# Kernel tuning notes

Measured on AMD Instinct MI355X. Metric: run time of the kernel, lower is better.

## Reference

```python
import jax, jax.numpy as jnp
import numpy as np
import math

B, W, BINS, BANDS = 2, 2048, 1024, 8  # cropsize == W
HEAD = BINS // BANDS


def setup_inputs() -> dict:
    key = jax.random.key(0)
    ks = jax.random.split(key, 10)
    s = 1.0 / math.sqrt(BINS)
    return {
        "x": jax.random.normal(ks[0], (B, W, BINS), jnp.float32),
        "Wq": jax.random.normal(ks[1], (BINS, BINS), jnp.float32) * s,
        "bq": jax.random.normal(ks[2], (BINS,), jnp.float32) * s,
        "Wk": jax.random.normal(ks[3], (BINS, BINS), jnp.float32) * s,
        "bk": jax.random.normal(ks[4], (BINS,), jnp.float32) * s,
        "Wv": jax.random.normal(ks[5], (BINS, BINS), jnp.float32) * s,
        "bv": jax.random.normal(ks[6], (BINS,), jnp.float32) * s,
        "Wo": jax.random.normal(ks[7], (BINS, BINS), jnp.float32) * s,
        "bo": jax.random.normal(ks[8], (BINS,), jnp.float32) * s,
        "er": jax.random.normal(ks[9], (HEAD, W), jnp.float32) * s,  # [bins//num_bands, cropsize]
    }


def reference(x, Wq, bq, Wk, bk, Wv, bv, Wo, bo, er):
    b, w, h = x.shape
    n = BANDS
    # projections -> [b, n, w, head]
    q = (x @ Wq.T + bq).reshape(b, w, n, -1).transpose(0, 2, 1, 3)
    k = (x @ Wk.T + bk).reshape(b, w, n, -1).transpose(0, 2, 1, 3)
    v = (x @ Wv.T + bv).reshape(b, w, n, -1).transpose(0, 2, 1, 3)
    # relative position bias via skew trick: [b, n, w, cropsize]
    qer = jnp.einsum('bnwd,dc->bnwc', q, er)
    p = jnp.pad(qer, ((0, 0), (0, 0), (0, 0), (1, 0)))  # pad left of last dim
    p = jnp.swapaxes(p, 2, 3)[:, :, 1:, :]              # [b, n, w, w]
    a = (jnp.einsum('bnqd,bnkd->bnqk', q, k) + p) / math.sqrt(h)
    attn = jax.nn.softmax(a, axis=-1)
    ctx = jnp.einsum('bnqk,bnkd->bnqd', attn, v).transpose(0, 2, 1, 3).reshape(b, w, h)
    o = ctx @ Wo.T + bo
    return (o, a)
```

## Files before the change

kernel.cpp:

```cpp
#include <hip/hip_runtime.h>

typedef __attribute__((ext_vector_type(8))) __bf16 bf16x8;
typedef __attribute__((ext_vector_type(4))) float f32x4;

__device__ __forceinline__ unsigned short f2bf(float f) {
  __bf16 h = (__bf16)f;
  return __builtin_bit_cast(unsigned short, h);
}

__device__ __forceinline__ f32x4 mfma_bf16(bf16x8 a, bf16x8 b, f32x4 c) {
  return __builtin_amdgcn_mfma_f32_16x16x32_bf16(a, b, c, 0, 0, 0);
}

__device__ __forceinline__ void gload_lds16(const void* g, void* l) {
  __builtin_amdgcn_global_load_lds((const __attribute__((address_space(1))) void*)g,
                                   (__attribute__((address_space(3))) void*)l, 16, 0, 0);
}


__global__ void cvt_f32_bf16(const float* __restrict__ in, unsigned short* __restrict__ out, int n4) {
  int i = blockIdx.x * blockDim.x + threadIdx.x;
  if (i < n4) {
    float4 v = reinterpret_cast<const float4*>(in)[i];
    ushort4 o;
    o.x = f2bf(v.x); o.y = f2bf(v.y); o.z = f2bf(v.z); o.w = f2bf(v.w);
    reinterpret_cast<ushort4*>(out)[i] = o;
  }
}

__global__ void cvt4_f32_bf16(const float* __restrict__ a, const float* __restrict__ b,
                              const float* __restrict__ c, const float* __restrict__ d,
                              unsigned short* __restrict__ oa, unsigned short* __restrict__ ob,
                              unsigned short* __restrict__ oc, unsigned short* __restrict__ od) {
  int i = blockIdx.x * blockDim.x + threadIdx.x;
  int which = i >> 18, j = i & 262143;
  const float* src = (which == 0) ? a : (which == 1) ? b : (which == 2) ? c : d;
  unsigned short* dst = (which == 0) ? oa : (which == 1) ? ob : (which == 2) ? oc : od;
  float4 v = reinterpret_cast<const float4*>(src)[j];
  ushort4 o;
  o.x = f2bf(v.x); o.y = f2bf(v.y); o.z = f2bf(v.z); o.w = f2bf(v.w);
  reinterpret_cast<ushort4*>(dst)[j] = o;
}

__global__ void er_transpose(const float* __restrict__ er, unsigned short* __restrict__ ert) {
  __shared__ float t[32][33];
  int w0 = blockIdx.x * 32, d0 = blockIdx.y * 32;
  int tx = threadIdx.x, ty = threadIdx.y;
#pragma unroll
  for (int i = 0; i < 4; ++i)
    t[ty + i * 8][tx] = er[(size_t)(d0 + ty + i * 8) * 2048 + w0 + tx];
  __syncthreads();
#pragma unroll
  for (int i = 0; i < 4; ++i)
    ert[(size_t)(w0 + ty + i * 8) * 128 + d0 + tx] = f2bf(t[tx][ty + i * 8]);
}


__device__ __forceinline__ void gemm_tile(
    const unsigned short* __restrict__ A,
    const unsigned short* __restrict__ Bt,
    const float* __restrict__ bias,
    void* __restrict__ C,
    int mode, int i0, int j0,
    unsigned short* lds)
{
  char* base = (char*)lds;

  const int tid = threadIdx.x;
  const int lane = tid & 63, wid = tid >> 6;
  const int lr = lane & 15, lq = lane >> 4;
  const int wr = wid >> 1, wc = wid & 1;

  f32x4 acc[4][4] = {};

  const int srow = tid >> 2;
  const int scolb = (tid & 3) << 4;

  const char* Abase = (const char*)A + (size_t)(i0 + srow) * 2048 + scolb;
  const char* Bbase = (const char*)Bt + (size_t)(j0 + srow) * 2048 + scolb;

  gload_lds16(Abase,             base + tid * 16);
  gload_lds16(Abase + 64 * 2048, base + 4096 + tid * 16);
  gload_lds16(Bbase,             base + 8192 + tid * 16);
  gload_lds16(Bbase + 64 * 2048, base + 12288 + tid * 16);

  for (int kt = 0; kt < 32; ++kt) {
    char* cbuf = base + (kt & 1) * 16384;
    char* nbuf = base + ((kt + 1) & 1) * 16384;

    asm volatile("s_waitcnt vmcnt(0)" ::: "memory");
    __builtin_amdgcn_sched_barrier(0);
    __builtin_amdgcn_s_barrier();
    __builtin_amdgcn_sched_barrier(0);

    if (kt < 31) {
      const int k0b = (kt + 1) * 64;
      gload_lds16(Abase + k0b,             nbuf + tid * 16);
      gload_lds16(Abase + k0b + 64 * 2048, nbuf + 4096 + tid * 16);
      gload_lds16(Bbase + k0b,             nbuf + 8192 + tid * 16);
      gload_lds16(Bbase + k0b + 64 * 2048, nbuf + 12288 + tid * 16);
    }
    __builtin_amdgcn_sched_barrier(0);

    bf16x8 af[4], bfr[4];
#pragma unroll
    for (int m = 0; m < 4; ++m)
      af[m] = *(const bf16x8*)(cbuf + (wr * 64 + m * 16 + lr) * 64 + lq * 16);
#pragma unroll
    for (int n = 0; n < 4; ++n)
      bfr[n] = *(const bf16x8*)(cbuf + 8192 + (wc * 64 + n * 16 + lr) * 64 + lq * 16);
    __builtin_amdgcn_s_setprio(1);
#pragma unroll
    for (int m = 0; m < 4; ++m)
#pragma unroll
      for (int n = 0; n < 4; ++n)
        acc[m][n] = mfma_bf16(af[m], bfr[n], acc[m][n]);
    __builtin_amdgcn_s_setprio(0);
  }

  float bv[4];
#pragma unroll
  for (int n = 0; n < 4; ++n) bv[n] = bias[j0 + wc * 64 + n * 16 + lr];

  if (mode == 1) {
    __syncthreads();
#pragma unroll
    for (int m = 0; m < 4; ++m)
#pragma unroll
      for (int n = 0; n < 4; ++n)
#pragma unroll
        for (int r = 0; r < 4; ++r) {
          int il = wr * 64 + m * 16 + lq * 4 + r;
          int jl = wc * 64 + n * 16 + lr;
          lds[jl * 132 + il] = f2bf(acc[m][n][r] + bv[n]);
        }
    __syncthreads();
    const int b = i0 >> 11, w0 = i0 & 2047, bd = j0 >> 7;
    unsigned short* out = (unsigned short*)C;
    for (int idx = tid; idx < 16384; idx += 256) {
      int dl = idx >> 7, wl = idx & 127;
      out[(size_t)((b * 8 + bd) * 128 + dl) * 2048 + w0 + wl] = lds[dl * 132 + wl];
    }
  } else if (mode == 0) {
    unsigned short* out = (unsigned short*)C;
#pragma unroll
    for (int m = 0; m < 4; ++m)
#pragma unroll
      for (int n = 0; n < 4; ++n)
#pragma unroll
        for (int r = 0; r < 4; ++r) {
          int gi = i0 + wr * 64 + m * 16 + lq * 4 + r;
          int gj = j0 + wc * 64 + n * 16 + lr;
          out[(size_t)gi * 1024 + gj] = f2bf(acc[m][n][r] + bv[n]);
        }
  } else {
    float* out = (float*)C;
#pragma unroll
    for (int m = 0; m < 4; ++m)
#pragma unroll
      for (int n = 0; n < 4; ++n)
#pragma unroll
        for (int r = 0; r < 4; ++r) {
          int gi = i0 + wr * 64 + m * 16 + lq * 4 + r;
          int gj = j0 + wc * 64 + n * 16 + lr;
          out[(size_t)gi * 1024 + gj] = acc[m][n][r] + bv[n];
        }
  }
}

__global__ __launch_bounds__(256, 2) void gemm_qkv(
    const unsigned short* __restrict__ xb,
    const unsigned short* __restrict__ Wqb, const unsigned short* __restrict__ Wkb,
    const unsigned short* __restrict__ Wvb,
    const float* __restrict__ bq, const float* __restrict__ bk, const float* __restrict__ bv_,
    unsigned short* __restrict__ Qb, unsigned short* __restrict__ Kb,
    unsigned short* __restrict__ Vtb)
{
  __shared__ unsigned short lds[16896];
  const int which = blockIdx.y >> 3;
  const int i0 = blockIdx.x * 128, j0 = (blockIdx.y & 7) * 128;
  const unsigned short* Bt = (which == 0) ? Wqb : (which == 1) ? Wkb : Wvb;
  const float* bias = (which == 0) ? bq : (which == 1) ? bk : bv_;
  void* C = (which == 0) ? (void*)Qb : (which == 1) ? (void*)Kb : (void*)Vtb;
  gemm_tile(xb, Bt, bias, C, (which == 2) ? 1 : 0, i0, j0, lds);
}

__global__ __launch_bounds__(256, 2) void gemm_bt(
    const unsigned short* __restrict__ A,
    const unsigned short* __restrict__ Bt,
    const float* __restrict__ bias,
    void* __restrict__ C,
    int mode)
{
  __shared__ unsigned short lds[16896];
  gemm_tile(A, Bt, bias, C, mode, blockIdx.x * 128, blockIdx.y * 128, lds);
}


__global__ __launch_bounds__(512) void attn_fused(
    const unsigned short* __restrict__ Qb,
    const unsigned short* __restrict__ Kb,
    const unsigned short* __restrict__ Vt,
    const unsigned short* __restrict__ ErT,
    float* __restrict__ a_out,
    unsigned short* __restrict__ ctx)
{
  __shared__ __align__(16) char Klb[32768];
  __shared__ __align__(16) char Qlb[32768];
  __shared__ __align__(16) char Vlb[32768];
  __shared__ __align__(16) char Plb[32768];

  const int bb = blockIdx.x;
  const int bd = bb & 7, b = bb >> 3;
  const int qi0 = blockIdx.y * 128;
  const int tid = threadIdx.x, wid = tid >> 6, lane = tid & 63;
  const int lr = lane & 15, lq = lane >> 4;

  bf16x8 qf[4], ef[4];
  {
    const unsigned short* Qrow = Qb + (size_t)(b * 2048 + qi0 + wid * 16 + lr) * 1024 + bd * 128;
    const unsigned short* Erow = ErT + (size_t)(qi0 + wid * 16 + lr) * 128;
#pragma unroll
    for (int kk = 0; kk < 4; ++kk) {
      qf[kk] = *(const bf16x8*)(Qrow + kk * 32 + lq * 8);
      ef[kk] = *(const bf16x8*)(Erow + kk * 32 + lq * 8);
    }
  }

  int ldso[4];
  const char *ksrc[4], *qsrc[4], *vsrc[4];
#pragma unroll
  for (int p = 0; p < 4; ++p) {
    int L = p * 8192 + tid * 16;
    int row = L >> 8, cs = L & 255;
    int sc = cs ^ ((row & 7) << 4);
    ldso[p] = L;
    ksrc[p] = (const char*)Kb + ((size_t)(b * 2048 + row) * 1024 + bd * 128) * 2 + sc;
    qsrc[p] = (const char*)Qb + ((size_t)(b * 2048 + row) * 1024 + bd * 128) * 2 + sc;
    vsrc[p] = (const char*)Vt + ((size_t)(bb * 128 + row) * 2048) * 2 + sc;
  }

#pragma unroll
  for (int p = 0; p < 4; ++p) gload_lds16(ksrc[p], Klb + ldso[p]);
#pragma unroll
  for (int p = 0; p < 4; ++p) gload_lds16(qsrc[p], Qlb + ldso[p]);
#pragma unroll
  for (int p = 0; p < 4; ++p) gload_lds16(vsrc[p], Vlb + ldso[p]);

  f32x4 oacc[8] = {};
  float M[4], L[4];
#pragma unroll
  for (int r = 0; r < 4; ++r) { M[r] = -1e30f; L[r] = 0.f; }

  float* abase = a_out + (size_t)bb * 2048 * 2048;

  for (int kt = 0; kt < 16; ++kt) {
    const int kj0 = kt * 128;
    const size_t nkq = (size_t)((kt + 1) & 15) * 262144;
    const size_t nv = (size_t)((kt + 1) & 15) * 256;

    asm volatile("s_waitcnt vmcnt(4)" ::: "memory");
    __builtin_amdgcn_sched_barrier(0);
    __builtin_amdgcn_s_barrier();
    __builtin_amdgcn_sched_barrier(0);

    f32x4 sacc[8] = {};
    __builtin_amdgcn_s_setprio(1);
#pragma unroll
    for (int kk = 0; kk < 4; ++kk) {
#pragma unroll
      for (int nf = 0; nf < 8; ++nf) {
        const int row = nf * 16 + lr;
        bf16x8 kf = *(const bf16x8*)(Klb + row * 256 + ((kk * 64 + lq * 16) ^ ((row & 7) << 4)));
        sacc[nf] = mfma_bf16(qf[kk], kf, sacc[nf]);
      }
#pragma unroll
      for (int nf = 0; nf < 8; ++nf) {
        const int row = nf * 16 + lr;
        bf16x8 qkf = *(const bf16x8*)(Qlb + row * 256 + ((kk * 64 + lq * 16) ^ ((row & 7) << 4)));
        sacc[nf] = mfma_bf16(ef[kk], qkf, sacc[nf]);
      }
    }
    __builtin_amdgcn_s_setprio(0);

    __builtin_amdgcn_sched_barrier(0);
    __builtin_amdgcn_s_barrier();
    __builtin_amdgcn_sched_barrier(0);

#pragma unroll
    for (int nf = 0; nf < 8; ++nf)
#pragma unroll
      for (int r = 0; r < 4; ++r) sacc[nf][r] *= 0.03125f;
    {
      const int qrow_base = qi0 + wid * 16 + lq * 4;
#pragma unroll
      for (int nf = 0; nf < 8; ++nf)
#pragma unroll
        for (int r = 0; r < 4; ++r)
          abase[(size_t)(qrow_base + r) * 2048 + kj0 + nf * 16 + lr] = sacc[nf][r];
    }

    __builtin_amdgcn_sched_barrier(0);
#pragma unroll
    for (int p = 0; p < 4; ++p) gload_lds16(ksrc[p] + nkq, Klb + ldso[p]);
#pragma unroll
    for (int p = 0; p < 4; ++p) gload_lds16(qsrc[p] + nkq, Qlb + ldso[p]);
    __builtin_amdgcn_sched_barrier(0);

    float rmax[4];
#pragma unroll
    for (int r = 0; r < 4; ++r) {
      float m0 = sacc[0][r];
#pragma unroll
      for (int nf = 1; nf < 8; ++nf) m0 = fmaxf(m0, sacc[nf][r]);
      m0 = fmaxf(m0, __shfl_xor(m0, 1));
      m0 = fmaxf(m0, __shfl_xor(m0, 2));
      m0 = fmaxf(m0, __shfl_xor(m0, 4));
      m0 = fmaxf(m0, __shfl_xor(m0, 8));
      rmax[r] = m0;
    }
    bool small = (rmax[0] - M[0] <= 8.f) & (rmax[1] - M[1] <= 8.f) &
                 (rmax[2] - M[2] <= 8.f) & (rmax[3] - M[3] <= 8.f);
    unsigned long long vote = __ballot(small);
    if (vote != ~0ull) {
      float scl[4];
#pragma unroll
      for (int r = 0; r < 4; ++r) {
        float Mn = fmaxf(M[r], rmax[r]);
        scl[r] = __expf(M[r] - Mn);
        M[r] = Mn;
        L[r] *= scl[r];
      }
#pragma unroll
      for (int dn = 0; dn < 8; ++dn)
#pragma unroll
        for (int r = 0; r < 4; ++r) oacc[dn][r] *= scl[r];
    }
    float rsum[4] = {0.f, 0.f, 0.f, 0.f};
#pragma unroll
    for (int nf = 0; nf < 8; ++nf)
#pragma unroll
      for (int r = 0; r < 4; ++r) {
        float pv = __expf(sacc[nf][r] - M[r]);
        sacc[nf][r] = pv;
        rsum[r] += pv;
      }
    {
      const int prow0 = wid * 16 + lq * 4;
#pragma unroll
      for (int nf = 0; nf < 8; ++nf)
#pragma unroll
        for (int r = 0; r < 4; ++r) {
          const int row = prow0 + r;
          *(unsigned short*)(Plb + row * 256 + (((nf * 16 + lr) * 2) ^ ((row & 7) << 4))) =
              f2bf(sacc[nf][r]);
        }
    }
#pragma unroll
    for (int r = 0; r < 4; ++r) {
      rsum[r] += __shfl_xor(rsum[r], 1);
      rsum[r] += __shfl_xor(rsum[r], 2);
      rsum[r] += __shfl_xor(rsum[r], 4);
      rsum[r] += __shfl_xor(rsum[r], 8);
      L[r] += rsum[r];
    }

    asm volatile("s_waitcnt vmcnt(8)" ::: "memory");
    __builtin_amdgcn_sched_barrier(0);

    __builtin_amdgcn_s_setprio(1);
#pragma unroll
    for (int kk = 0; kk < 4; ++kk) {
      const int prow = wid * 16 + lr;
      bf16x8 pf = *(const bf16x8*)(Plb + prow * 256 + ((kk * 64 + lq * 16) ^ ((prow & 7) << 4)));
#pragma unroll
      for (int dn = 0; dn < 8; ++dn) {
        const int vrow = dn * 16 + lr;
        bf16x8 vf = *(const bf16x8*)(Vlb + vrow * 256 + ((kk * 64 + lq * 16) ^ ((vrow & 7) << 4)));
        oacc[dn] = mfma_bf16(pf, vf, oacc[dn]);
      }
    }
    __builtin_amdgcn_s_setprio(0);

    __builtin_amdgcn_sched_barrier(0);
    __builtin_amdgcn_s_barrier();
    __builtin_amdgcn_sched_barrier(0);
#pragma unroll
    for (int p = 0; p < 4; ++p) gload_lds16(vsrc[p] + nv, Vlb + ldso[p]);
    __builtin_amdgcn_sched_barrier(0);
  }

  {
    const int qrow_base = b * 2048 + qi0 + wid * 16 + lq * 4;
#pragma unroll
    for (int dn = 0; dn < 8; ++dn)
#pragma unroll
      for (int r = 0; r < 4; ++r) {
        float v = oacc[dn][r] / L[r];
        ctx[(size_t)(qrow_base + r) * 1024 + bd * 128 + dn * 16 + lr] = f2bf(v);
      }
  }
}


extern "C" void kernel_launch(void* const* d_in, const int* in_sizes, int n_in,
                              void* d_out, int out_size, void* d_ws, size_t ws_size,
                              hipStream_t stream) {
  const float* x  = (const float*)d_in[0];
  const float* Wq = (const float*)d_in[1];
  const float* bq = (const float*)d_in[2];
  const float* Wk = (const float*)d_in[3];
  const float* bk = (const float*)d_in[4];
  const float* Wv = (const float*)d_in[5];
  const float* bv = (const float*)d_in[6];
  const float* Wo = (const float*)d_in[7];
  const float* bo = (const float*)d_in[8];
  const float* er = (const float*)d_in[9];

  char* ws = (char*)d_ws;
  unsigned short* xb  = (unsigned short*)(ws + 0);
  unsigned short* Wqb = (unsigned short*)(ws + 8388608);
  unsigned short* Wkb = (unsigned short*)(ws + 10485760);
  unsigned short* Wvb = (unsigned short*)(ws + 12582912);
  unsigned short* Wob = (unsigned short*)(ws + 14680064);
  unsigned short* Qb  = (unsigned short*)(ws + 16777216);
  unsigned short* Kb  = (unsigned short*)(ws + 25165824);
  unsigned short* Vtb = (unsigned short*)(ws + 33554432);
  unsigned short* ctx = (unsigned short*)(ws + 41943040);
  unsigned short* ert = (unsigned short*)(ws + 50331648);

  float* a_out = (float*)d_out + 4194304;

  cvt_f32_bf16<<<dim3(4096), dim3(256), 0, stream>>>(x, xb, 1048576);
  cvt4_f32_bf16<<<dim3(4096), dim3(256), 0, stream>>>(Wq, Wk, Wv, Wo, Wqb, Wkb, Wvb, Wob);
  er_transpose<<<dim3(64, 4), dim3(32, 8), 0, stream>>>(er, ert);

  gemm_qkv<<<dim3(32, 24), dim3(256), 0, stream>>>(xb, Wqb, Wkb, Wvb, bq, bk, bv,
                                                   Qb, Kb, Vtb);

  attn_fused<<<dim3(16, 16), dim3(512), 0, stream>>>(Qb, Kb, Vtb, ert, a_out, ctx);

  gemm_bt<<<dim3(32, 8), dim3(256), 0, stream>>>(ctx, Wob, bo, d_out, 2);
}
```

Measured before the change: 188.6 us.

## Split attention over key halves with 32-row warps and add merge kernel

Each attention block now handles 256 query rows (32 per warp, two MFMA fragments) over one half of the keys. This doubles reuse of each K/Q/V LDS tile per load, and LDS use is cut by sharing one buffer between K/Q and P. Partial outputs and per-row max/sum are written to workspace, and a new merge kernel combines the two halves into ctx. The cost is an extra kernel launch, an extra bf16 round trip of partial outputs, and loss of the earlier cross-iteration prefetch overlap, since loads now wait with vmcnt(0) and are issued only after PV. Register pressure also rises.

After: 322.0 us, median of 3. 1.71x slower.

```diff
diff --git a/kernel.cpp b/kernel.cpp
--- a/kernel.cpp
+++ b/kernel.cpp
@@ -6,6 +6,11 @@
 __device__ __forceinline__ unsigned short f2bf(float f) {
   __bf16 h = (__bf16)f;
   return __builtin_bit_cast(unsigned short, h);
+}
+
+__device__ __forceinline__ float bf2f(unsigned short u) {
+  unsigned int x = ((unsigned int)u) << 16;
+  return __builtin_bit_cast(float, x);
 }
 
 __device__ __forceinline__ f32x4 mfma_bf16(bf16x8 a, bf16x8 b, f32x4 c) {
@@ -203,27 +208,30 @@
     const unsigned short* __restrict__ Vt,
     const unsigned short* __restrict__ ErT,
     float* __restrict__ a_out,
-    unsigned short* __restrict__ ctx)
+    unsigned short* __restrict__ Opart,
+    float* __restrict__ MLp)
 {
-  __shared__ __align__(16) char Klb[32768];
-  __shared__ __align__(16) char Qlb[32768];
+  __shared__ __align__(16) char KQlb[65536];
   __shared__ __align__(16) char Vlb[32768];
-  __shared__ __align__(16) char Plb[32768];
 
   const int bb = blockIdx.x;
   const int bd = bb & 7, b = bb >> 3;
-  const int qi0 = blockIdx.y * 128;
+  const int qt = blockIdx.y >> 1, kh = blockIdx.y & 1;
+  const int qi0 = qt * 256;
+  const int kbase = kh * 1024;
   const int tid = threadIdx.x, wid = tid >> 6, lane = tid & 63;
   const int lr = lane & 15, lq = lane >> 4;
 
-  bf16x8 qf[4], ef[4];
-  {
-    const unsigned short* Qrow = Qb + (size_t)(b * 2048 + qi0 + wid * 16 + lr) * 1024 + bd * 128;
-    const unsigned short* Erow = ErT + (size_t)(qi0 + wid * 16 + lr) * 128;
+  bf16x8 qf[2][4], ef[2][4];
+#pragma unroll
+  for (int fr = 0; fr < 2; ++fr) {
+    const unsigned short* Qrow =
+        Qb + (size_t)(b * 2048 + qi0 + wid * 32 + fr * 16 + lr) * 1024 + bd * 128;
+    const unsigned short* Erow = ErT + (size_t)(qi0 + wid * 32 + fr * 16 + lr) * 128;
 #pragma unroll
     for (int kk = 0; kk < 4; ++kk) {
-      qf[kk] = *(const bf16x8*)(Qrow + kk * 32 + lq * 8);
-      ef[kk] = *(const bf16x8*)(Erow + kk * 32 + lq * 8);
+      qf[fr][kk] = *(const bf16x8*)(Qrow + kk * 32 + lq * 8);
+      ef[fr][kk] = *(const bf16x8*)(Erow + kk * 32 + lq * 8);
     }
   }
 
@@ -231,153 +239,153 @@
   const char *ksrc[4], *qsrc[4], *vsrc[4];
 #pragma unroll
   for (int p = 0; p < 4; ++p) {
-    int L = p * 8192 + tid * 16;
-    int row = L >> 8, cs = L & 255;
+    int Lo = p * 8192 + tid * 16;
+    int row = Lo >> 8, cs = Lo & 255;
     int sc = cs ^ ((row & 7) << 4);
-    ldso[p] = L;
-    ksrc[p] = (const char*)Kb + ((size_t)(b * 2048 + row) * 1024 + bd * 128) * 2 + sc;
-    qsrc[p] = (const char*)Qb + ((size_t)(b * 2048 + row) * 1024 + bd * 128) * 2 + sc;
-    vsrc[p] = (const char*)Vt + ((size_t)(bb * 128 + row) * 2048) * 2 + sc;
-  }
-
-#pragma unroll
-  for (int p = 0; p < 4; ++p) gload_lds16(ksrc[p], Klb + ldso[p]);
-#pragma unroll
-  for (int p = 0; p < 4; ++p) gload_lds16(qsrc[p], Qlb + ldso[p]);
+    ldso[p] = Lo;
+    ksrc[p] = (const char*)Kb + ((size_t)(b * 2048 + kbase + row) * 1024 + bd * 128) * 2 + sc;
+    qsrc[p] = (const char*)Qb + ((size_t)(b * 2048 + kbase + row) * 1024 + bd * 128) * 2 + sc;
+    vsrc[p] = (const char*)Vt + ((size_t)(bb * 128 + row) * 2048 + kbase) * 2 + sc;
+  }
+#pragma unroll
+  for (int p = 0; p < 4; ++p) gload_lds16(ksrc[p], KQlb + ldso[p]);
+#pragma unroll
+  for (int p = 0; p < 4; ++p) gload_lds16(qsrc[p], KQlb + 32768 + ldso[p]);
 #pragma unroll
   for (int p = 0; p < 4; ++p) gload_lds16(vsrc[p], Vlb + ldso[p]);
 
-  f32x4 oacc[8] = {};
-  float M[4], L[4];
-#pragma unroll
-  for (int r = 0; r < 4; ++r) { M[r] = -1e30f; L[r] = 0.f; }
-
-  float* abase = a_out + (size_t)bb * 2048 * 2048;
-
-  for (int kt = 0; kt < 16; ++kt) {
-    const int kj0 = kt * 128;
-    const size_t nkq = (size_t)((kt + 1) & 15) * 262144;
-    const size_t nv = (size_t)((kt + 1) & 15) * 256;
-
-    asm volatile("s_waitcnt vmcnt(4)" ::: "memory");
+  f32x4 oacc[2][8] = {};
+  float M[2][4], Ls[2][4];
+#pragma unroll
+  for (int fr = 0; fr < 2; ++fr)
+#pragma unroll
+    for (int r = 0; r < 4; ++r) { M[fr][r] = -1e30f; Ls[fr][r] = 0.f; }
+
+  float* abase = a_out + (size_t)bb * 4194304;
+
+  for (int kt = 0; kt < 8; ++kt) {
+    asm volatile("s_waitcnt vmcnt(0)" ::: "memory");
     __builtin_amdgcn_sched_barrier(0);
     __builtin_amdgcn_s_barrier();
     __builtin_amdgcn_sched_barrier(0);
 
-    f32x4 sacc[8] = {};
+    f32x4 sacc[2][8] = {};
     __builtin_amdgcn_s_setprio(1);
 #pragma unroll
     for (int kk = 0; kk < 4; ++kk) {
 #pragma unroll
       for (int nf = 0; nf < 8; ++nf) {
         const int row = nf * 16 + lr;
-        bf16x8 kf = *(const bf16x8*)(Klb + row * 256 + ((kk * 64 + lq * 16) ^ ((row & 7) << 4)));
-        sacc[nf] = mfma_bf16(qf[kk], kf, sacc[nf]);
+        const int coff = (kk * 64 + lq * 16) ^ ((row & 7) << 4);
+        bf16x8 kf = *(const bf16x8*)(KQlb + row * 256 + coff);
+        sacc[0][nf] = mfma_bf16(qf[0][kk], kf, sacc[0][nf]);
+        sacc[1][nf] = mfma_bf16(qf[1][kk], kf, sacc[1][nf]);
+        bf16x8 qkf = *(const bf16x8*)(KQlb + 32768 + row * 256 + coff);
+        sacc[0][nf] = mfma_bf16(ef[0][kk], qkf, sacc[0][nf]);
+        sacc[1][nf] = mfma_bf16(ef[1][kk], qkf, sacc[1][nf]);
       }
-#pragma unroll
-      for (int nf = 0; nf < 8; ++nf) {
-        const int row = nf * 16 + lr;
-        bf16x8 qkf = *(const bf16x8*)(Qlb + row * 256 + ((kk * 64 + lq * 16) ^ ((row & 7) << 4)));
-        sacc[nf] = mfma_bf16(ef[kk], qkf, sacc[nf]);
+    }
+    __builtin_amdgcn_s_setprio(0);
+
+    __builtin_amdgcn_sched_barrier(0);
+    __builtin_amdgcn_s_barrier();
+    __builtin_amdgcn_sched_barrier(0);
+
+    const int kcol0 = kbase + kt * 128;
+#pragma unroll
+    for (int fr = 0; fr < 2; ++fr) {
+#pragma unroll
+      for (int nf = 0; nf < 8; ++nf)
+#pragma unroll
+        for (int r = 0; r < 4; ++r) sacc[fr][nf][r] *= 0.03125f;
+      const int qrow_base = qi0 + wid * 32 + fr * 16 + lq * 4;
+#pragma unroll
+      for (int nf = 0; nf < 8; ++nf)
+#pragma unroll
+        for (int r = 0; r < 4; ++r)
+          abase[(size_t)(qrow_base + r) * 2048 + kcol0 + nf * 16 + lr] = sacc[fr][nf][r];
+    }
+
+    float rmax[2][4];
+#pragma unroll
+    for (int fr = 0; fr < 2; ++fr)
+#pragma unroll
+      for (int r = 0; r < 4; ++r) {
+        float m0 = sacc[fr][0][r];
+#pragma unroll
+        for (int nf = 1; nf < 8; ++nf) m0 = fmaxf(m0, sacc[fr][nf][r]);
+        m0 = fmaxf(m0, __shfl_xor(m0, 1));
+        m0 = fmaxf(m0, __shfl_xor(m0, 2));
+        m0 = fmaxf(m0, __shfl_xor(m0, 4));
+        m0 = fmaxf(m0, __shfl_xor(m0, 8));
+        rmax[fr][r] = m0;
       }
-    }
-    __builtin_amdgcn_s_setprio(0);
-
-    __builtin_amdgcn_sched_barrier(0);
-    __builtin_amdgcn_s_barrier();
-    __builtin_amdgcn_sched_barrier(0);
-
-#pragma unroll
-    for (int nf = 0; nf < 8; ++nf)
-#pragma unroll
-      for (int r = 0; r < 4; ++r) sacc[nf][r] *= 0.03125f;
-    {
-      const int qrow_base = qi0 + wid * 16 + lq * 4;
-#pragma unroll
-      for (int nf = 0; nf < 8; ++nf)
-#pragma unroll
-        for (int r = 0; r < 4; ++r)
-          abase[(size_t)(qrow_base + r) * 2048 + kj0 + nf * 16 + lr] = sacc[nf][r];
-    }
-
-    __builtin_amdgcn_sched_barrier(0);
-#pragma unroll
-    for (int p = 0; p < 4; ++p) gload_lds16(ksrc[p] + nkq, Klb + ldso[p]);
-#pragma unroll
-    for (int p = 0; p < 4; ++p) gload_lds16(qsrc[p] + nkq, Qlb + ldso[p]);
-    __builtin_amdgcn_sched_barrier(0);
-
-    float rmax[4];
-#pragma unroll
-    for (int r = 0; r < 4; ++r) {
-      float m0 = sacc[0][r];
-#pragma unroll
-      for (int nf = 1; nf < 8; ++nf) m0 = fmaxf(m0, sacc[nf][r]);
-      m0 = fmaxf(m0, __shfl_xor(m0, 1));
-      m0 = fmaxf(m0, __shfl_xor(m0, 2));
-      m0 = fmaxf(m0, __shfl_xor(m0, 4));
-      m0 = fmaxf(m0, __shfl_xor(m0, 8));
-      rmax[r] = m0;
-    }
-    bool small = (rmax[0] - M[0] <= 8.f) & (rmax[1] - M[1] <= 8.f) &
-                 (rmax[2] - M[2] <= 8.f) & (rmax[3] - M[3] <= 8.f);
+    bool small = true;
+#pragma unroll
+    for (int fr = 0; fr < 2; ++fr)
+#pragma unroll
+      for (int r = 0; r < 4; ++r) small &= (rmax[fr][r] - M[fr][r] <= 8.f);
     unsigned long long vote = __ballot(small);
     if (vote != ~0ull) {
-      float scl[4];
+#pragma unroll
+      for (int fr = 0; fr < 2; ++fr) {
+        float scl[4];
+#pragma unroll
+        for (int r = 0; r < 4; ++r) {
+          float Mn = fmaxf(M[fr][r], rmax[fr][r]);
+          scl[r] = __expf(M[fr][r] - Mn);
+          M[fr][r] = Mn;
+          Ls[fr][r] *= scl[r];
+        }
+#pragma unroll
+        for (int dn = 0; dn < 8; ++dn)
+#pragma unroll
+          for (int r = 0; r < 4; ++r) oacc[fr][dn][r] *= scl[r];
+      }
+    }
+#pragma unroll
+    for (int fr = 0; fr < 2; ++fr) {
+      float rsum[4] = {0.f, 0.f, 0.f, 0.f};
+#pragma unroll
+      for (int nf = 0; nf < 8; ++nf)
+#pragma unroll
+        for (int r = 0; r < 4; ++r) {
+          float pv = __expf(sacc[fr][nf][r] - M[fr][r]);
+          sacc[fr][nf][r] = pv;
+          rsum[r] += pv;
+        }
+      const int prow0 = wid * 32 + fr * 16 + lq * 4;
+#pragma unroll
+      for (int nf = 0; nf < 8; ++nf)
+#pragma unroll
+        for (int r = 0; r < 4; ++r) {
+          const int row = prow0 + r;
+          *(unsigned short*)(KQlb + row * 256 + (((nf * 16 + lr) * 2) ^ ((row & 7) << 4))) =
+              f2bf(sacc[fr][nf][r]);
+        }
 #pragma unroll
       for (int r = 0; r < 4; ++r) {
-        float Mn = fmaxf(M[r], rmax[r]);
-        scl[r] = __expf(M[r] - Mn);
-        M[r] = Mn;
-        L[r] *= scl[r];
+        rsum[r] += __shfl_xor(rsum[r], 1);
+        rsum[r] += __shfl_xor(rsum[r], 2);
+        rsum[r] += __shfl_xor(rsum[r], 4);
+        rsum[r] += __shfl_xor(rsum[r], 8);
+        Ls[fr][r] += rsum[r];
       }
-#pragma unroll
-      for (int dn = 0; dn < 8; ++dn)
-#pragma unroll
-        for (int r = 0; r < 4; ++r) oacc[dn][r] *= scl[r];
-    }
-    float rsum[4] = {0.f, 0.f, 0.f, 0.f};
-#pragma unroll
-    for (int nf = 0; nf < 8; ++nf)
-#pragma unroll
-      for (int r = 0; r < 4; ++r) {
-        float pv = __expf(sacc[nf][r] - M[r]);
-        sacc[nf][r] = pv;
-        rsum[r] += pv;
-      }
-    {
-      const int prow0 = wid * 16 + lq * 4;
-#pragma unroll
-      for (int nf = 0; nf < 8; ++nf)
-#pragma unroll
-        for (int r = 0; r < 4; ++r) {
-          const int row = prow0 + r;
-          *(unsigned short*)(Plb + row * 256 + (((nf * 16 + lr) * 2) ^ ((row & 7) << 4))) =
-              f2bf(sacc[nf][r]);
-        }
-    }
-#pragma unroll
-    for (int r = 0; r < 4; ++r) {
-      rsum[r] += __shfl_xor(rsum[r], 1);
-      rsum[r] += __shfl_xor(rsum[r], 2);
-      rsum[r] += __shfl_xor(rsum[r], 4);
-      rsum[r] += __shfl_xor(rsum[r], 8);
-      L[r] += rsum[r];
-    }
-
-    asm volatile("s_waitcnt vmcnt(8)" ::: "memory");
-    __builtin_amdgcn_sched_barrier(0);
+    }
 
     __builtin_amdgcn_s_setprio(1);
 #pragma unroll
     for (int kk = 0; kk < 4; ++kk) {
-      const int prow = wid * 16 + lr;
-      bf16x8 pf = *(const bf16x8*)(Plb + prow * 256 + ((kk * 64 + lq * 16) ^ ((prow & 7) << 4)));
+      const int pr0 = wid * 32 + lr;
+      const int pr1 = pr0 + 16;
+      bf16x8 pf0 = *(const bf16x8*)(KQlb + pr0 * 256 + ((kk * 64 + lq * 16) ^ ((pr0 & 7) << 4)));
+      bf16x8 pf1 = *(const bf16x8*)(KQlb + pr1 * 256 + ((kk * 64 + lq * 16) ^ ((pr1 & 7) << 4)));
 #pragma unroll
       for (int dn = 0; dn < 8; ++dn) {
         const int vrow = dn * 16 + lr;
         bf16x8 vf = *(const bf16x8*)(Vlb + vrow * 256 + ((kk * 64 + lq * 16) ^ ((vrow & 7) << 4)));
-        oacc[dn] = mfma_bf16(pf, vf, oacc[dn]);
+        oacc[0][dn] = mfma_bf16(pf0, vf, oacc[0][dn]);
+        oacc[1][dn] = mfma_bf16(pf1, vf, oacc[1][dn]);
       }
     }
     __builtin_amdgcn_s_setprio(0);
@@ -385,20 +393,65 @@
     __builtin_amdgcn_sched_barrier(0);
     __builtin_amdgcn_s_barrier();
     __builtin_amdgcn_sched_barrier(0);
-#pragma unroll
-    for (int p = 0; p < 4; ++p) gload_lds16(vsrc[p] + nv, Vlb + ldso[p]);
+    if (kt < 7) {
+      const size_t ko = (size_t)(kt + 1) * 262144;
+      const size_t vo = (size_t)(kt + 1) * 256;
+#pragma unroll
+      for (int p = 0; p < 4; ++p) gload_lds16(ksrc[p] + ko, KQlb + ldso[p]);
+#pragma unroll
+      for (int p = 0; p < 4; ++p) gload_lds16(qsrc[p] + ko, KQlb + 32768 + ldso[p]);
+#pragma unroll
+      for (int p = 0; p < 4; ++p) gload_lds16(vsrc[p] + vo, Vlb + ldso[p]);
+    }
     __builtin_amdgcn_sched_barrier(0);
   }
 
   {
-    const int qrow_base = b * 2048 + qi0 + wid * 16 + lq * 4;
-#pragma unroll
-    for (int dn = 0; dn < 8; ++dn)
-#pragma unroll
-      for (int r = 0; r < 4; ++r) {
-        float v = oacc[dn][r] / L[r];
-        ctx[(size_t)(qrow_base + r) * 1024 + bd * 128 + dn * 16 + lr] = f2bf(v);
+    const int g = (bb * 8 + qt) * 2 + kh;
+    unsigned short* Ob = Opart + (size_t)g * 32768;
+    float* mlb = MLp + (size_t)g * 512;
+#pragma unroll
+    for (int fr = 0; fr < 2; ++fr) {
+#pragma unroll
+      for (int dn = 0; dn < 8; ++dn)
+#pragma unroll
+        for (int r = 0; r < 4; ++r) {
+          int row = wid * 32 + fr * 16 + lq * 4 + r;
+          Ob[row * 128 + dn * 16 + lr] = f2bf(oacc[fr][dn][r]);
+        }
+      if (lr == 0) {
+#pragma unroll
+        for (int r = 0; r < 4; ++r) {
+          int row = wid * 32 + fr * 16 + lq * 4 + r;
+          mlb[row * 2] = M[fr][r];
+          mlb[row * 2 + 1] = Ls[fr][r];
+        }
       }
+    }
+  }
+}
+
+__global__ __launch_bounds__(256) void attn_merge(
+    const unsigned short* __restrict__ Opart,
+    const float* __restrict__ MLp,
+    unsigned short* __restrict__ ctx)
+{
+  const int bb = blockIdx.x, qt = blockIdx.y;
+  const int b = bb >> 3, bd = bb & 7;
+  const int g = (bb * 8 + qt) * 2;
+  const unsigned short* O0 = Opart + (size_t)g * 32768;
+  const unsigned short* O1 = O0 + 32768;
+  const float* ml0 = MLp + (size_t)g * 512;
+  const float* ml1 = ml0 + 512;
+  for (int idx = threadIdx.x; idx < 32768; idx += 256) {
+    int row = idx >> 7, d = idx & 127;
+    float M0 = ml0[row * 2], L0 = ml0[row * 2 + 1];
+    float M1 = ml1[row * 2], L1 = ml1[row * 2 + 1];
+    float Mn = fmaxf(M0, M1);
+    float s0 = __expf(M0 - Mn), s1 = __expf(M1 - Mn);
+    float Ln = L0 * s0 + L1 * s1;
+    float o = (bf2f(O0[idx]) * s0 + bf2f(O1[idx]) * s1) / Ln;
+    ctx[(size_t)(b * 2048 + qt * 256 + row) * 1024 + bd * 128 + d] = f2bf(o);
   }
 }
 
@@ -418,16 +471,18 @@
   const float* er = (const float*)d_in[9];
 
   char* ws = (char*)d_ws;
-  unsigned short* xb  = (unsigned short*)(ws + 0);
-  unsigned short* Wqb = (unsigned short*)(ws + 8388608);
-  unsigned short* Wkb = (unsigned short*)(ws + 10485760);
-  unsigned short* Wvb = (unsigned short*)(ws + 12582912);
-  unsigned short* Wob = (unsigned short*)(ws + 14680064);
-  unsigned short* Qb  = (unsigned short*)(ws + 16777216);
-  unsigned short* Kb  = (unsigned short*)(ws + 25165824);
-  unsigned short* Vtb = (unsigned short*)(ws + 33554432);
-  unsigned short* ctx = (unsigned short*)(ws + 41943040);
-  unsigned short* ert = (unsigned short*)(ws + 50331648);
+  unsigned short* xb    = (unsigned short*)(ws + 0);
+  unsigned short* Wqb   = (unsigned short*)(ws + 8388608);
+  unsigned short* Wkb   = (unsigned short*)(ws + 10485760);
+  unsigned short* Wvb   = (unsigned short*)(ws + 12582912);
+  unsigned short* Opart = (unsigned short*)(ws + 0);
+  unsigned short* Qb    = (unsigned short*)(ws + 16777216);
+  unsigned short* Kb    = (unsigned short*)(ws + 25165824);
+  unsigned short* Vtb   = (unsigned short*)(ws + 33554432);
+  unsigned short* ctx   = (unsigned short*)(ws + 41943040);
+  unsigned short* ert   = (unsigned short*)(ws + 50331648);
+  unsigned short* Wob   = (unsigned short*)(ws + 50855936);
+  float*          MLp   = (float*)(ws + 52953088);
 
   float* a_out = (float*)d_out + 4194304;
 
@@ -438,7 +493,8 @@
   gemm_qkv<<<dim3(32, 24), dim3(256), 0, stream>>>(xb, Wqb, Wkb, Wvb, bq, bk, bv,
                                                    Qb, Kb, Vtb);
 
-  attn_fused<<<dim3(16, 16), dim3(512), 0, stream>>>(Qb, Kb, Vtb, ert, a_out, ctx);
+  attn_fused<<<dim3(16, 16), dim3(512), 0, stream>>>(Qb, Kb, Vtb, ert, a_out, Opart, MLp);
+  attn_merge<<<dim3(16, 8), dim3(256), 0, stream>>>(Opart, MLp, ctx);
 
   gemm_bt<<<dim3(32, 8), dim3(256), 0, stream>>>(ctx, Wob, bo, d_out, 2);
 }
```

## Halve attention block threads so each wave handles two query row fragments

Applied to the files above, without the earlier changes.

The fused attention kernel now runs 256 threads (4 waves) per block instead of 512, and each wave computes 32 query rows as two 16-row fragments. Each K, Q-skew and V fragment read from LDS is reused across two MFMAs, cutting LDS read traffic per MFMA. Async copy counts per thread double and the wait counts are adjusted to match. A barrier is added before the P·V stage. The cost is roughly double the accumulator and fragment register use per wave, with fewer waves to hide latency.

Result: slower. 216.9 us (+15.0%).

```diff
diff --git a/kernel.cpp b/kernel.cpp
--- a/kernel.cpp
+++ b/kernel.cpp
@@ -197,7 +197,7 @@
 }
 
 
-__global__ __launch_bounds__(512) void attn_fused(
+__global__ __launch_bounds__(256, 1) void attn_fused(
     const unsigned short* __restrict__ Qb,
     const unsigned short* __restrict__ Kb,
     const unsigned short* __restrict__ Vt,
@@ -216,22 +216,24 @@
   const int tid = threadIdx.x, wid = tid >> 6, lane = tid & 63;
   const int lr = lane & 15, lq = lane >> 4;
 
-  bf16x8 qf[4], ef[4];
-  {
-    const unsigned short* Qrow = Qb + (size_t)(b * 2048 + qi0 + wid * 16 + lr) * 1024 + bd * 128;
-    const unsigned short* Erow = ErT + (size_t)(qi0 + wid * 16 + lr) * 128;
+  bf16x8 qf[2][4], ef[2][4];
+#pragma unroll
+  for (int fr = 0; fr < 2; ++fr) {
+    const unsigned short* Qrow =
+        Qb + (size_t)(b * 2048 + qi0 + wid * 32 + fr * 16 + lr) * 1024 + bd * 128;
+    const unsigned short* Erow = ErT + (size_t)(qi0 + wid * 32 + fr * 16 + lr) * 128;
 #pragma unroll
     for (int kk = 0; kk < 4; ++kk) {
-      qf[kk] = *(const bf16x8*)(Qrow + kk * 32 + lq * 8);
-      ef[kk] = *(const bf16x8*)(Erow + kk * 32 + lq * 8);
-    }
-  }
-
-  int ldso[4];
-  const char *ksrc[4], *qsrc[4], *vsrc[4];
-#pragma unroll
-  for (int p = 0; p < 4; ++p) {
-    int L = p * 8192 + tid * 16;
+      qf[fr][kk] = *(const bf16x8*)(Qrow + kk * 32 + lq * 8);
+      ef[fr][kk] = *(const bf16x8*)(Erow + kk * 32 + lq * 8);
+    }
+  }
+
+  int ldso[8];
+  const char *ksrc[8], *qsrc[8], *vsrc[8];
+#pragma unroll
+  for (int p = 0; p < 8; ++p) {
+    int L = p * 4096 + tid * 16;
     int row = L >> 8, cs = L & 255;
     int sc = cs ^ ((row & 7) << 4);
     ldso[p] = L;
@@ -241,16 +243,18 @@
   }
 
 #pragma unroll
-  for (int p = 0; p < 4; ++p) gload_lds16(ksrc[p], Klb + ldso[p]);
-#pragma unroll
-  for (int p = 0; p < 4; ++p) gload_lds16(qsrc[p], Qlb + ldso[p]);
-#pragma unroll
-  for (int p = 0; p < 4; ++p) gload_lds16(vsrc[p], Vlb + ldso[p]);
-
-  f32x4 oacc[8] = {};
-  float M[4], L[4];
-#pragma unroll
-  for (int r = 0; r < 4; ++r) { M[r] = -1e30f; L[r] = 0.f; }
+  for (int p = 0; p < 8; ++p) gload_lds16(ksrc[p], Klb + ldso[p]);
+#pragma unroll
+  for (int p = 0; p < 8; ++p) gload_lds16(qsrc[p], Qlb + ldso[p]);
+#pragma unroll
+  for (int p = 0; p < 8; ++p) gload_lds16(vsrc[p], Vlb + ldso[p]);
+
+  f32x4 oacc[2][8] = {};
+  float M[2][4], Ls[2][4];
+#pragma unroll
+  for (int fr = 0; fr < 2; ++fr)
+#pragma unroll
+    for (int r = 0; r < 4; ++r) { M[fr][r] = -1e30f; Ls[fr][r] = 0.f; }
 
   float* abase = a_out + (size_t)bb * 2048 * 2048;
 
@@ -259,26 +263,25 @@
     const size_t nkq = (size_t)((kt + 1) & 15) * 262144;
     const size_t nv = (size_t)((kt + 1) & 15) * 256;
 
-    asm volatile("s_waitcnt vmcnt(4)" ::: "memory");
+    asm volatile("s_waitcnt vmcnt(8)" ::: "memory");
     __builtin_amdgcn_sched_barrier(0);
     __builtin_amdgcn_s_barrier();
     __builtin_amdgcn_sched_barrier(0);
 
-    f32x4 sacc[8] = {};
+    f32x4 sacc[2][8] = {};
     __builtin_amdgcn_s_setprio(1);
 #pragma unroll
     for (int kk = 0; kk < 4; ++kk) {
 #pragma unroll
       for (int nf = 0; nf < 8; ++nf) {
         const int row = nf * 16 + lr;
-        bf16x8 kf = *(const bf16x8*)(Klb + row * 256 + ((kk * 64 + lq * 16) ^ ((row & 7) << 4)));
-        sacc[nf] = mfma_bf16(qf[kk], kf, sacc[nf]);
-      }
-#pragma unroll
-      for (int nf = 0; nf < 8; ++nf) {
-        const int row = nf * 16 + lr;
-        bf16x8 qkf = *(const bf16x8*)(Qlb + row * 256 + ((kk * 64 + lq * 16) ^ ((row & 7) << 4)));
-        sacc[nf] = mfma_bf16(ef[kk], qkf, sacc[nf]);
+        const int coff = (kk * 64 + lq * 16) ^ ((row & 7) << 4);
+        bf16x8 kf = *(const bf16x8*)(Klb + row * 256 + coff);
+        sacc[0][nf] = mfma_bf16(qf[0][kk], kf, sacc[0][nf]);
+        sacc[1][nf] = mfma_bf16(qf[1][kk], kf, sacc[1][nf]);
+        bf16x8 qkf = *(const bf16x8*)(Qlb + row * 256 + coff);
+        sacc[0][nf] = mfma_bf16(ef[0][kk], qkf, sacc[0][nf]);
+        sacc[1][nf] = mfma_bf16(ef[1][kk], qkf, sacc[1][nf]);
       }
     }
     __builtin_amdgcn_s_setprio(0);
@@ -288,96 +291,111 @@
     __builtin_amdgcn_sched_barrier(0);
 
 #pragma unroll
-    for (int nf = 0; nf < 8; ++nf)
-#pragma unroll
-      for (int r = 0; r < 4; ++r) sacc[nf][r] *= 0.03125f;
-    {
-      const int qrow_base = qi0 + wid * 16 + lq * 4;
+    for (int fr = 0; fr < 2; ++fr) {
 #pragma unroll
       for (int nf = 0; nf < 8; ++nf)
 #pragma unroll
+        for (int r = 0; r < 4; ++r) sacc[fr][nf][r] *= 0.03125f;
+      const int qrow_base = qi0 + wid * 32 + fr * 16 + lq * 4;
+#pragma unroll
+      for (int nf = 0; nf < 8; ++nf)
+#pragma unroll
         for (int r = 0; r < 4; ++r)
-          abase[(size_t)(qrow_base + r) * 2048 + kj0 + nf * 16 + lr] = sacc[nf][r];
-    }
-
-    __builtin_amdgcn_sched_barrier(0);
-#pragma unroll
-    for (int p = 0; p < 4; ++p) gload_lds16(ksrc[p] + nkq, Klb + ldso[p]);
-#pragma unroll
-    for (int p = 0; p < 4; ++p) gload_lds16(qsrc[p] + nkq, Qlb + ldso[p]);
-    __builtin_amdgcn_sched_barrier(0);
-
-    float rmax[4];
-#pragma unroll
-    for (int r = 0; r < 4; ++r) {
-      float m0 = sacc[0][r];
-#pragma unroll
-      for (int nf = 1; nf < 8; ++nf) m0 = fmaxf(m0, sacc[nf][r]);
-      m0 = fmaxf(m0, __shfl_xor(m0, 1));
-      m0 = fmaxf(m0, __shfl_xor(m0, 2));
-      m0 = fmaxf(m0, __shfl_xor(m0, 4));
-      m0 = fmaxf(m0, __shfl_xor(m0, 8));
-      rmax[r] = m0;
-    }
-    bool small = (rmax[0] - M[0] <= 8.f) & (rmax[1] - M[1] <= 8.f) &
-                 (rmax[2] - M[2] <= 8.f) & (rmax[3] - M[3] <= 8.f);
+          abase[(size_t)(qrow_base + r) * 2048 + kj0 + nf * 16 + lr] = sacc[fr][nf][r];
+    }
+
+    __builtin_amdgcn_sched_barrier(0);
+#pragma unroll
+    for (int p = 0; p < 8; ++p) gload_lds16(ksrc[p] + nkq, Klb + ldso[p]);
+#pragma unroll
+    for (int p = 0; p < 8; ++p) gload_lds16(qsrc[p] + nkq, Qlb + ldso[p]);
+    __builtin_amdgcn_sched_barrier(0);
+
+    float rmax[2][4];
+#pragma unroll
+    for (int fr = 0; fr < 2; ++fr)
+#pragma unroll
+      for (int r = 0; r < 4; ++r) {
+        float m0 = sacc[fr][0][r];
+#pragma unroll
+        for (int nf = 1; nf < 8; ++nf) m0 = fmaxf(m0, sacc[fr][nf][r]);
+        m0 = fmaxf(m0, __shfl_xor(m0, 1));
+        m0 = fmaxf(m0, __shfl_xor(m0, 2));
+        m0 = fmaxf(m0, __shfl_xor(m0, 4));
+        m0 = fmaxf(m0, __shfl_xor(m0, 8));
+        rmax[fr][r] = m0;
+      }
+    bool small = true;
+#pragma unroll
+    for (int fr = 0; fr < 2; ++fr)
+#pragma unroll
+      for (int r = 0; r < 4; ++r) small &= (rmax[fr][r] - M[fr][r] <= 8.f);
     unsigned long long vote = __ballot(small);
     if (vote != ~0ull) {
-      float scl[4];
-#pragma unroll
-      for (int r = 0; r < 4; ++r) {
-        float Mn = fmaxf(M[r], rmax[r]);
-        scl[r] = __expf(M[r] - Mn);
-        M[r] = Mn;
-        L[r] *= scl[r];
-      }
-#pragma unroll
-      for (int dn = 0; dn < 8; ++dn)
-#pragma unroll
-        for (int r = 0; r < 4; ++r) oacc[dn][r] *= scl[r];
-    }
-    float rsum[4] = {0.f, 0.f, 0.f, 0.f};
-#pragma unroll
-    for (int nf = 0; nf < 8; ++nf)
-#pragma unroll
-      for (int r = 0; r < 4; ++r) {
-        float pv = __expf(sacc[nf][r] - M[r]);
-        sacc[nf][r] = pv;
-        rsum[r] += pv;
-      }
-    {
-      const int prow0 = wid * 16 + lq * 4;
+#pragma unroll
+      for (int fr = 0; fr < 2; ++fr) {
+        float scl[4];
+#pragma unroll
+        for (int r = 0; r < 4; ++r) {
+          float Mn = fmaxf(M[fr][r], rmax[fr][r]);
+          scl[r] = __expf(M[fr][r] - Mn);
+          M[fr][r] = Mn;
+          Ls[fr][r] *= scl[r];
+        }
+#pragma unroll
+        for (int dn = 0; dn < 8; ++dn)
+#pragma unroll
+          for (int r = 0; r < 4; ++r) oacc[fr][dn][r] *= scl[r];
+      }
+    }
+#pragma unroll
+    for (int fr = 0; fr < 2; ++fr) {
+      float rsum[4] = {0.f, 0.f, 0.f, 0.f};
+#pragma unroll
+      for (int nf = 0; nf < 8; ++nf)
+#pragma unroll
+        for (int r = 0; r < 4; ++r) {
+          float pv = __expf(sacc[fr][nf][r] - M[fr][r]);
+          sacc[fr][nf][r] = pv;
+          rsum[r] += pv;
+        }
+      const int prow0 = wid * 32 + fr * 16 + lq * 4;
 #pragma unroll
       for (int nf = 0; nf < 8; ++nf)
 #pragma unroll
         for (int r = 0; r < 4; ++r) {
           const int row = prow0 + r;
           *(unsigned short*)(Plb + row * 256 + (((nf * 16 + lr) * 2) ^ ((row & 7) << 4))) =
-              f2bf(sacc[nf][r]);
-        }
-    }
-#pragma unroll
-    for (int r = 0; r < 4; ++r) {
-      rsum[r] += __shfl_xor(rsum[r], 1);
-      rsum[r] += __shfl_xor(rsum[r], 2);
-      rsum[r] += __shfl_xor(rsum[r], 4);
-      rsum[r] += __shfl_xor(rsum[r], 8);
-      L[r] += rsum[r];
-    }
-
-    asm volatile("s_waitcnt vmcnt(8)" ::: "memory");
+              f2bf(sacc[fr][nf][r]);
+        }
+#pragma unroll
+      for (int r = 0; r < 4; ++r) {
+        rsum[r] += __shfl_xor(rsum[r], 1);
+        rsum[r] += __shfl_xor(rsum[r], 2);
+        rsum[r] += __shfl_xor(rsum[r], 4);
+        rsum[r] += __shfl_xor(rsum[r], 8);
+        Ls[fr][r] += rsum[r];
+      }
+    }
+
+    asm volatile("s_waitcnt vmcnt(16)" ::: "memory");
+    __builtin_amdgcn_sched_barrier(0);
+    __builtin_amdgcn_s_barrier();
     __builtin_amdgcn_sched_barrier(0);
 
     __builtin_amdgcn_s_setprio(1);
 #pragma unroll
     for (int kk = 0; kk < 4; ++kk) {
-      const int prow = wid * 16 + lr;
-      bf16x8 pf = *(const bf16x8*)(Plb + prow * 256 + ((kk * 64 + lq * 16) ^ ((prow & 7) << 4)));
+      const int pr0 = wid * 32 + lr;
+      const int pr1 = pr0 + 16;
+      bf16x8 pf0 = *(const bf16x8*)(Plb + pr0 * 256 + ((kk * 64 + lq * 16) ^ ((pr0 & 7) << 4)));
+      bf16x8 pf1 = *(const bf16x8*)(Plb + pr1 * 256 + ((kk * 64 + lq * 16) ^ ((pr1 & 7) << 4)));
 #pragma unroll
       for (int dn = 0; dn < 8; ++dn) {
         const int vrow = dn * 16 + lr;
         bf16x8 vf = *(const bf16x8*)(Vlb + vrow * 256 + ((kk * 64 + lq * 16) ^ ((vrow & 7) << 4)));
-        oacc[dn] = mfma_bf16(pf, vf, oacc[dn]);
+        oacc[0][dn] = mfma_bf16(pf0, vf, oacc[0][dn]);
+        oacc[1][dn] = mfma_bf16(pf1, vf, oacc[1][dn]);
       }
     }
     __builtin_amdgcn_s_setprio(0);
@@ -386,17 +404,18 @@
     __builtin_amdgcn_s_barrier();
     __builtin_amdgcn_sched_barrier(0);
 #pragma unroll
-    for (int p = 0; p < 4; ++p) gload_lds16(vsrc[p] + nv, Vlb + ldso[p]);
-    __builtin_amdgcn_sched_barrier(0);
-  }
-
-  {
-    const int qrow_base = b * 2048 + qi0 + wid * 16 + lq * 4;
+    for (int p = 0; p < 8; ++p) gload_lds16(vsrc[p] + nv, Vlb + ldso[p]);
+    __builtin_amdgcn_sched_barrier(0);
+  }
+
+#pragma unroll
+  for (int fr = 0; fr < 2; ++fr) {
+    const int qrow_base = b * 2048 + qi0 + wid * 32 + fr * 16 + lq * 4;
 #pragma unroll
     for (int dn = 0; dn < 8; ++dn)
 #pragma unroll
       for (int r = 0; r < 4; ++r) {
-        float v = oacc[dn][r] / L[r];
+        float v = oacc[fr][dn][r] / Ls[fr][r];
         ctx[(size_t)(qrow_base + r) * 1024 + bd * 128 + dn * 16 + lr] = f2bf(v);
       }
   }
@@ -438,7 +457,7 @@
   gemm_qkv<<<dim3(32, 24), dim3(256), 0, stream>>>(xb, Wqb, Wkb, Wvb, bq, bk, bv,
                                                    Qb, Kb, Vtb);
 
-  attn_fused<<<dim3(16, 16), dim3(512), 0, stream>>>(Qb, Kb, Vtb, ert, a_out, ctx);
+  attn_fused<<<dim3(16, 16), dim3(256), 0, stream>>>(Qb, Kb, Vtb, ert, a_out, ctx);
 
   gemm_bt<<<dim3(32, 8), dim3(256), 0, stream>>>(ctx, Wob, bo, d_out, 2);
 }
```
